# Kernel tuning notes

Measured on AMD Instinct MI355X. Metric: run time of the kernel, lower is better.

The kernel has to match this reference:

```python
import jax, jax.numpy as jnp
import numpy as np

B, D, H, O, E = 8192, 1024, 4096, 1024, 3

def setup_inputs() -> dict:
    key = jax.random.key(0)
    ks = jax.random.split(key, 8)
    s = lambda fan_in: 1.0 / np.sqrt(fan_in)
    return {
        "x":   jax.random.normal(ks[0], (B, D), jnp.float32),
        "gw1": jax.random.normal(ks[1], (D, 256), jnp.float32) * s(D),
        "gb1": jnp.zeros((256,), jnp.float32),
        "gw2": jax.random.normal(ks[2], (256, 128), jnp.float32) * s(256),
        "gb2": jnp.zeros((128,), jnp.float32),
        "gw3": jax.random.normal(ks[3], (128, E), jnp.float32) * s(128),
        "gb3": jnp.zeros((E,), jnp.float32),
        "ew1": jax.random.normal(ks[4], (E, D, H), jnp.float32) * s(D),
        "eb1": jnp.zeros((E, H), jnp.float32),
        "ew2": jax.random.normal(ks[5], (E, H, O), jnp.float32) * s(H),
        "eb2": jnp.zeros((E, O), jnp.float32),
        "top_k": 2,
    }

def reference(x, gw1, gb1, gw2, gb2, gw3, gb3, ew1, eb1, ew2, eb2, top_k):
    # Gating network (dropout is identity in eval mode)
    g = jax.nn.relu(x @ gw1 + gb1)
    g = jax.nn.relu(g @ gw2 + gb2)
    gates = jax.nn.softmax(g @ gw3 + gb3, axis=-1)          # [B, E]

    # top-k routing with renormalized weights
    topk_scores, topk_idx = jax.lax.top_k(gates, top_k)     # [B, k]
    topk_scores = topk_scores / jnp.sum(topk_scores, axis=-1, keepdims=True)

    # scatter normalized scores into dense [B, E] combine weights
    b_ix = jnp.arange(x.shape[0])[:, None]
    combine = jnp.zeros_like(gates).at[b_ix, topk_idx].add(topk_scores)  # [B, E]

    # run all experts densely (small E=3), combine with routing weights
    eh = jax.nn.relu(jnp.einsum('bd,edh->beh', x, ew1) + eb1[None])      # [B, E, H]
    eo = jnp.einsum('beh,eho->beo', eh, ew2) + eb2[None]                 # [B, E, O]
    out = jnp.einsum('be,beo->bo', combine, eo)                          # [B, O]
    return out, gates
```

## Files before the change

### kernel.cpp

```cpp
#include <hip/hip_runtime.h>
#include <cstdint>
#include <cstddef>

#define B_ROWS 8192
#define D_DIM  1024
#define H_DIM  4096
#define O_DIM  1024
#define E_NUM  3
#define K2     (2 * H_DIM)
#define MT256  34
#define SLOT_MAX (MT256 * 256)

typedef __attribute__((ext_vector_type(4))) float f4;
typedef __attribute__((ext_vector_type(8))) _Float16 half8;

__device__ __forceinline__ unsigned short f2h_bits(float f) {
  _Float16 h = (_Float16)f;
  return __builtin_bit_cast(unsigned short, h);
}

__device__ __forceinline__ void async16(const void* g, void* l) {
  __builtin_amdgcn_global_load_lds(
      (const __attribute__((address_space(1))) unsigned int*)g,
      (__attribute__((address_space(3))) unsigned int*)l, 16, 0, 0);
}

__global__ __launch_bounds__(256) void k_cast_x(const float* __restrict__ in,
                                                unsigned short* __restrict__ out) {
  size_t i = (size_t)blockIdx.x * 256 + threadIdx.x;
  const f4* p = (const f4*)in;
  f4 a = p[2 * i], b = p[2 * i + 1];
  half8 h;
#pragma unroll
  for (int j = 0; j < 4; ++j) { h[j] = (_Float16)a[j]; h[4 + j] = (_Float16)b[j]; }
  *(half8*)(out + 8 * i) = h;
}

__global__ __launch_bounds__(256) void k_transpose_cast(const float* __restrict__ in,
                                                        unsigned short* __restrict__ out,
                                                        int R, int C) {
  __shared__ float tile[32][33];
  const size_t eoff = (size_t)blockIdx.z * R * C;
  const float* I = in + eoff;
  unsigned short* O = out + eoff;
  int c0 = blockIdx.x * 32, r0 = blockIdx.y * 32;
  int tx = threadIdx.x & 31, ty = threadIdx.x >> 5;
#pragma unroll
  for (int i = 0; i < 4; ++i)
    tile[ty + 8 * i][tx] = I[(size_t)(r0 + ty + 8 * i) * C + c0 + tx];
  __syncthreads();
#pragma unroll
  for (int i = 0; i < 4; ++i)
    O[(size_t)(c0 + ty + 8 * i) * R + r0 + tx] = f2h_bits(tile[tx][ty + 8 * i]);
}

__global__ __launch_bounds__(256) void k_gemm_f32(const float* __restrict__ A,
                                                  const float* __restrict__ Bm,
                                                  const float* __restrict__ bias,
                                                  float* __restrict__ C,
                                                  int N, int K) {
  __shared__ float sAT[16][68];
  __shared__ float sB[16][68];
  const int t = threadIdx.x;
  const int tx = t & 15, ty = t >> 4;
  const int m0 = blockIdx.y * 64, n0 = blockIdx.x * 64;
  float acc[4][4] = {};
  for (int k0 = 0; k0 < K; k0 += 16) {
    __syncthreads();
#pragma unroll
    for (int i = 0; i < 4; ++i) {
      int idx = t + i * 256;
      int r = idx >> 4, c = idx & 15;
      sAT[c][r] = A[(size_t)(m0 + r) * K + (k0 + c)];
      int rb = idx >> 6, cb = idx & 63;
      sB[rb][cb] = Bm[(size_t)(k0 + rb) * N + (n0 + cb)];
    }
    __syncthreads();
#pragma unroll
    for (int kk = 0; kk < 16; ++kk) {
      f4 av = *(const f4*)&sAT[kk][ty * 4];
      f4 bv = *(const f4*)&sB[kk][tx * 4];
#pragma unroll
      for (int i = 0; i < 4; ++i)
#pragma unroll
        for (int j = 0; j < 4; ++j)
          acc[i][j] = fmaf(av[i], bv[j], acc[i][j]);
    }
  }
#pragma unroll
  for (int i = 0; i < 4; ++i) {
    int row = m0 + ty * 4 + i;
    f4 v;
#pragma unroll
    for (int j = 0; j < 4; ++j)
      v[j] = fmaxf(acc[i][j] + bias[n0 + tx * 4 + j], 0.f);
    *(f4*)&C[(size_t)row * N + n0 + tx * 4] = v;
  }
}

__global__ __launch_bounds__(256) void k_gate_topk(const float* __restrict__ h2,
                                                   const float* __restrict__ gw3,
                                                   const float* __restrict__ gb3,
                                                   float* __restrict__ gates,
                                                   float* __restrict__ combine,
                                                   int* __restrict__ bucket) {
  const int lane = threadIdx.x & 63;
  const int row = blockIdx.x * 4 + (threadIdx.x >> 6);
  const float* h = h2 + (size_t)row * 128;
  float h0 = h[lane], h1 = h[lane + 64];
  float l0 = h0 * gw3[lane * 3 + 0] + h1 * gw3[(lane + 64) * 3 + 0];
  float l1 = h0 * gw3[lane * 3 + 1] + h1 * gw3[(lane + 64) * 3 + 1];
  float l2 = h0 * gw3[lane * 3 + 2] + h1 * gw3[(lane + 64) * 3 + 2];
#pragma unroll
  for (int off = 32; off > 0; off >>= 1) {
    l0 += __shfl_down(l0, off);
    l1 += __shfl_down(l1, off);
    l2 += __shfl_down(l2, off);
  }
  if (lane == 0) {
    float g0 = l0 + gb3[0], g1v = l1 + gb3[1], g2v = l2 + gb3[2];
    float mx = fmaxf(g0, fmaxf(g1v, g2v));
    float e0 = expf(g0 - mx), e1 = expf(g1v - mx), e2 = expf(g2v - mx);
    float inv = 1.f / (e0 + e1 + e2);
    float p0 = e0 * inv, p1 = e1 * inv, p2 = e2 * inv;
    gates[row * 3 + 0] = p0; gates[row * 3 + 1] = p1; gates[row * 3 + 2] = p2;
    int amin = 0; float pm = p0;
    if (p1 <= pm) { pm = p1; amin = 1; }
    if (p2 <= pm) { pm = p2; amin = 2; }
    float denom = (p0 + p1 + p2) - pm;
    combine[row * 3 + 0] = (amin == 0) ? 0.f : p0 / denom;
    combine[row * 3 + 1] = (amin == 1) ? 0.f : p1 / denom;
    combine[row * 3 + 2] = (amin == 2) ? 0.f : p2 / denom;
    bucket[row] = amin;
  }
}

__global__ __launch_bounds__(256) void k_count(const int* __restrict__ bucket,
                                               int* __restrict__ cnt) {
  int row = blockIdx.x * 256 + threadIdx.x;
  int b = bucket[row];
  int lane = threadIdx.x & 63;
#pragma unroll
  for (int bid = 0; bid < 3; ++bid) {
    unsigned long long m = __ballot(b == bid);
    if (m && b == bid) {
      int prefix = __popcll(m & ((1ull << lane) - 1));
      if (prefix == 0) atomicAdd(&cnt[bid], __popcll(m));
    }
  }
}

__global__ void k_meta(const int* __restrict__ cnt, int* __restrict__ meta,
                       int* __restrict__ cnt2) {
  int t0 = (cnt[0] + 255) >> 8;
  int t1 = (cnt[1] + 255) >> 8;
  int t2 = (cnt[2] + 255) >> 8;
  meta[0] = 0; meta[1] = t0; meta[2] = t0 + t1; meta[3] = t0 + t1 + t2;
  cnt2[0] = 0; cnt2[1] = 0; cnt2[2] = 0;
}

__global__ __launch_bounds__(256) void k_scatter(const int* __restrict__ bucket,
                                                 const int* __restrict__ meta,
                                                 int* __restrict__ cnt2,
                                                 int* __restrict__ sorted) {
  int row = blockIdx.x * 256 + threadIdx.x;
  int b = bucket[row];
  int lane = threadIdx.x & 63;
#pragma unroll
  for (int bid = 0; bid < 3; ++bid) {
    unsigned long long m = __ballot(b == bid);
    if (m) {
      int cntm = __popcll(m);
      int leader = __ffsll((unsigned long long)m) - 1;
      int base = 0;
      if (lane == leader) base = atomicAdd(&cnt2[bid], cntm);
      base = __shfl(base, leader);
      if (b == bid) {
        int prefix = __popcll(m & ((1ull << lane) - 1));
        sorted[meta[bid] * 256 + base + prefix] = row;
      }
    }
  }
}

__device__ __forceinline__ void bucket_experts(int b, int& ea, int& eb) {
  ea = (b == 0) ? 1 : 0;
  eb = (b == 2) ? 1 : 2;
}


#define BAR8()  do { __builtin_amdgcn_s_barrier(); __builtin_amdgcn_sched_barrier(0); } while (0)
#define LGKM0() do { asm volatile("s_waitcnt lgkmcnt(0)" ::: "memory"); __builtin_amdgcn_sched_barrier(0); } while (0)
#define VMW(n)  do { asm volatile("s_waitcnt vmcnt(" #n ")" ::: "memory"); __builtin_amdgcn_sched_barrier(0); } while (0)

#define STG_A(buf, h, kt) do { \
    async16(aptr[(h) * 2 + 0] + (size_t)(kt) * 64, smem + (buf) * 32768 + (h) * 16384 + t * 16); \
    async16(aptr[(h) * 2 + 1] + (size_t)(kt) * 64, smem + (buf) * 32768 + (h) * 16384 + 8192 + t * 16); \
  } while (0)
#define STG_B(buf, h, kt) do { \
    async16(bptr[(h) * 2 + 0] + (size_t)(kt) * 64, smem + 65536 + (buf) * 32768 + (h) * 16384 + t * 16); \
    async16(bptr[(h) * 2 + 1] + (size_t)(kt) * 64, smem + 65536 + (buf) * 32768 + (h) * 16384 + 8192 + t * 16); \
  } while (0)
#define LDA8(buf, mh) do { \
    _Pragma("unroll") \
    for (int mf = 0; mf < 4; ++mf) { \
      fa[mf][0] = *(const half8*)(smem + (buf) * 32768 + baseA + (mh) * 8192 + mf * 2048 + ck0); \
      fa[mf][1] = *(const half8*)(smem + (buf) * 32768 + baseA + (mh) * 8192 + mf * 2048 + ck1); \
    } } while (0)
#define LDB8(buf, nh) do { \
    _Pragma("unroll") \
    for (int nf2 = 0; nf2 < 2; ++nf2) { \
      fb[(nh) * 2 + nf2][0] = *(const half8*)(smem + (buf) * 32768 + baseB + ((nh) * 2 + nf2) * 2048 + ck0); \
      fb[(nh) * 2 + nf2][1] = *(const half8*)(smem + (buf) * 32768 + baseB + ((nh) * 2 + nf2) * 2048 + ck1); \
    } } while (0)
#define MM8(mh, nh) do { \
    _Pragma("unroll") \
    for (int mf = 0; mf < 4; ++mf) { \
      _Pragma("unroll") \
      for (int nf2 = 0; nf2 < 2; ++nf2) { \
        acc[(mh) * 4 + mf][(nh) * 2 + nf2] = __builtin_amdgcn_mfma_f32_16x16x32_f16( \
            fa[mf][0], fb[(nh) * 2 + nf2][0], acc[(mh) * 4 + mf][(nh) * 2 + nf2], 0, 0, 0); \
        acc[(mh) * 4 + mf][(nh) * 2 + nf2] = __builtin_amdgcn_mfma_f32_16x16x32_f16( \
            fa[mf][1], fb[(nh) * 2 + nf2][1], acc[(mh) * 4 + mf][(nh) * 2 + nf2], 0, 0, 0); \
      } } } while (0)

#define KLOOP8(NITER, LASTKT) \
  _Pragma("unroll 1") \
  for (int it = 0; it < (NITER) - 1; ++it) { \
    const int kt = 2 * it; \
    LDA8(0, 0); LDB8(0, 0); STG_A(1, 0, kt + 1); \
    BAR8(); LGKM0(); \
    __builtin_amdgcn_s_setprio(1); MM8(0, 0); __builtin_amdgcn_s_setprio(0); \
    BAR8(); \
    LDB8(0, 1); STG_A(1, 1, kt + 1); \
    BAR8(); LGKM0(); \
    __builtin_amdgcn_s_setprio(1); MM8(0, 1); __builtin_amdgcn_s_setprio(0); \
    BAR8(); \
    LDA8(0, 1); STG_B(0, 0, kt + 2); \
    BAR8(); LGKM0(); \
    __builtin_amdgcn_s_setprio(1); MM8(1, 0); __builtin_amdgcn_s_setprio(0); \
    BAR8(); \
    STG_A(0, 0, kt + 2); \
    BAR8(); LGKM0(); \
    __builtin_amdgcn_s_setprio(1); MM8(1, 1); __builtin_amdgcn_s_setprio(0); \
    VMW(4); BAR8(); \
    LDA8(1, 0); LDB8(1, 0); STG_A(0, 1, kt + 2); \
    BAR8(); LGKM0(); \
    __builtin_amdgcn_s_setprio(1); MM8(0, 0); __builtin_amdgcn_s_setprio(0); \
    BAR8(); \
    LDB8(1, 1); STG_B(0, 1, kt + 2); \
    BAR8(); LGKM0(); \
    __builtin_amdgcn_s_setprio(1); MM8(0, 1); __builtin_amdgcn_s_setprio(0); \
    BAR8(); \
    LDA8(1, 1); STG_B(1, 0, kt + 3); \
    BAR8(); LGKM0(); \
    __builtin_amdgcn_s_setprio(1); MM8(1, 0); __builtin_amdgcn_s_setprio(0); \
    BAR8(); \
    STG_B(1, 1, kt + 3); \
    BAR8(); LGKM0(); \
    __builtin_amdgcn_s_setprio(1); MM8(1, 1); __builtin_amdgcn_s_setprio(0); \
    VMW(4); BAR8(); \
  } \
  {  \
    LDA8(0, 0); LDB8(0, 0); STG_A(1, 0, LASTKT); \
    BAR8(); LGKM0(); \
    __builtin_amdgcn_s_setprio(1); MM8(0, 0); __builtin_amdgcn_s_setprio(0); \
    BAR8(); \
    LDB8(0, 1); STG_A(1, 1, LASTKT); \
    BAR8(); LGKM0(); \
    __builtin_amdgcn_s_setprio(1); MM8(0, 1); __builtin_amdgcn_s_setprio(0); \
    BAR8(); \
    LDA8(0, 1); \
    BAR8(); LGKM0(); \
    __builtin_amdgcn_s_setprio(1); MM8(1, 0); __builtin_amdgcn_s_setprio(0); \
    BAR8(); \
    BAR8(); LGKM0(); \
    __builtin_amdgcn_s_setprio(1); MM8(1, 1); __builtin_amdgcn_s_setprio(0); \
    VMW(0); BAR8(); \
    LDA8(1, 0); LDB8(1, 0); MM8(0, 0); \
    LDB8(1, 1); MM8(0, 1); \
    LDA8(1, 1); MM8(1, 0); \
    MM8(1, 1); \
  }

__global__ __launch_bounds__(512, 2) void k_expert_h8(const unsigned short* __restrict__ Xh,
                                                      const unsigned short* __restrict__ W1T,
                                                      const float* __restrict__ combine,
                                                      const float* __restrict__ eb1,
                                                      const int* __restrict__ sorted,
                                                      const int* __restrict__ meta,
                                                      unsigned short* __restrict__ EHS) {
  constexpr int K = D_DIM;
  const int mt = blockIdx.x;
  const int tb1 = meta[1], tb2 = meta[2], tb3 = meta[3];
  if (mt >= tb3) return;
  const int b = (mt >= tb2) ? 2 : (mt >= tb1) ? 1 : 0;
  int ea, ebx; bucket_experts(b, ea, ebx);
  const int z = blockIdx.z;
  const int e = z ? ebx : ea;
  const int slot0 = mt * 256;
  const int n0 = blockIdx.y * 256;

  __shared__ __align__(16) char smem[131072];
  __shared__ float sC[256];
  const int t = threadIdx.x;
  if (t < 256) {
    int r = sorted[slot0 + t];
    sC[t] = (r < 0) ? 0.f : combine[(size_t)r * 3 + e];
  }

  const int jrow = t >> 3;
  const int j = (t & 7) ^ (jrow & 7);
  const unsigned short* aptr[4];
  const unsigned short* bptr[4];
#pragma unroll
  for (int i = 0; i < 4; ++i) {
    int R = jrow + i * 64;
    int r = sorted[slot0 + R];
    int rr = (r < 0) ? 0 : r;
    aptr[i] = Xh + (size_t)rr * K + j * 8;
    bptr[i] = W1T + (size_t)e * H_DIM * K + (size_t)(n0 + R) * K + j * 8;
  }
  const int lane = t & 63;
  const int wid = t >> 6;
  const int wm = wid >> 2, wn = wid & 3;
  const int quad = lane >> 4, l16 = lane & 15;
  const int ck0 = ((quad) ^ (l16 & 7)) * 16;
  const int ck1 = ((4 + quad) ^ (l16 & 7)) * 16;
  const int baseA = (wm * 128 + l16) * 128;
  const int baseB = 65536 + (wn * 64 + l16) * 128;

  f4 acc[8][4] = {};
  half8 fa[4][2], fb[4][2];

  STG_A(0, 0, 0); STG_A(0, 1, 0); STG_B(0, 0, 0); STG_B(0, 1, 0);
  STG_B(1, 0, 1); STG_B(1, 1, 1);
  VMW(4); BAR8();

  KLOOP8(8, 15)

  const float* bias = eb1 + (size_t)e * H_DIM;
#pragma unroll
  for (int nf = 0; nf < 4; ++nf) {
    int col = n0 + wn * 64 + nf * 16 + l16;
    float bb = bias[col];
#pragma unroll
    for (int mf = 0; mf < 8; ++mf) {
#pragma unroll
      for (int r = 0; r < 4; ++r) {
        int rloc = wm * 128 + mf * 16 + quad * 4 + r;
        float v = fmaxf(acc[mf][nf][r] + bb, 0.f) * sC[rloc];
        EHS[(size_t)(slot0 + rloc) * K2 + (size_t)z * H_DIM + col] = f2h_bits(v);
      }
    }
  }
}

__global__ __launch_bounds__(512, 2) void k_expert_o8(const unsigned short* __restrict__ EHS,
                                                      const unsigned short* __restrict__ W2T,
                                                      const float* __restrict__ combine,
                                                      const float* __restrict__ eb2,
                                                      const int* __restrict__ sorted,
                                                      const int* __restrict__ meta,
                                                      float* __restrict__ OUT) {
  const int mt = blockIdx.x;
  const int tb1 = meta[1], tb2 = meta[2], tb3 = meta[3];
  if (mt >= tb3) return;
  const int b = (mt >= tb2) ? 2 : (mt >= tb1) ? 1 : 0;
  int ea, ebx; bucket_experts(b, ea, ebx);
  const int hz = blockIdx.z;
  const int e = hz ? ebx : ea;
  const int slot0 = mt * 256;
  const int n0 = blockIdx.y * 256;

  __shared__ __align__(16) char smem[131072];
  __shared__ int sRow[256];
  __shared__ float sCa[256], sCb[256];
  const int t = threadIdx.x;
  if (t < 256) {
    int r = sorted[slot0 + t];
    sRow[t] = r;
    int rr = (r < 0) ? 0 : r;
    sCa[t] = combine[(size_t)rr * 3 + ea];
    sCb[t] = combine[(size_t)rr * 3 + ebx];
  }

  const int jrow = t >> 3;
  const int j = (t & 7) ^ (jrow & 7);
  const unsigned short* aptr[4];
  const unsigned short* bptr[4];
#pragma unroll
  for (int i = 0; i < 4; ++i) {
    int R = jrow + i * 64;
    int r = sorted[slot0 + R];
    int rr = (r < 0) ? 0 : r;
    aptr[i] = EHS + (size_t)(slot0 + R) * K2 + (size_t)hz * H_DIM + j * 8;
    (void)rr;
    bptr[i] = W2T + (size_t)e * O_DIM * H_DIM + (size_t)(n0 + R) * H_DIM + j * 8;
  }
  const int lane = t & 63;
  const int wid = t >> 6;
  const int wm = wid >> 2, wn = wid & 3;
  const int quad = lane >> 4, l16 = lane & 15;
  const int ck0 = ((quad) ^ (l16 & 7)) * 16;
  const int ck1 = ((4 + quad) ^ (l16 & 7)) * 16;
  const int baseA = (wm * 128 + l16) * 128;
  const int baseB = 65536 + (wn * 64 + l16) * 128;

  f4 acc[8][4] = {};
  half8 fa[4][2], fb[4][2];

  STG_A(0, 0, 0); STG_A(0, 1, 0); STG_B(0, 0, 0); STG_B(0, 1, 0);
  STG_B(1, 0, 1); STG_B(1, 1, 1);
  VMW(4); BAR8();

  KLOOP8(32, 63)

#pragma unroll
  for (int nf = 0; nf < 4; ++nf) {
    int col = n0 + wn * 64 + nf * 16 + l16;
    float ba = eb2[(size_t)ea * O_DIM + col];
    float bb = eb2[(size_t)ebx * O_DIM + col];
#pragma unroll
    for (int mf = 0; mf < 8; ++mf) {
#pragma unroll
      for (int r = 0; r < 4; ++r) {
        int rloc = wm * 128 + mf * 16 + quad * 4 + r;
        int rowg = sRow[rloc];
        if (rowg >= 0) {
          float v = acc[mf][nf][r];
          if (hz == 0) v += sCa[rloc] * ba + sCb[rloc] * bb;
          atomicAdd(&OUT[(size_t)rowg * O_DIM + col], v);
        }
      }
    }
  }
}

extern "C" void kernel_launch(void* const* d_in, const int* in_sizes, int n_in,
                              void* d_out, int out_size, void* d_ws, size_t ws_size,
                              hipStream_t stream) {
  const float* x   = (const float*)d_in[0];
  const float* gw1 = (const float*)d_in[1];
  const float* gb1 = (const float*)d_in[2];
  const float* gw2 = (const float*)d_in[3];
  const float* gb2 = (const float*)d_in[4];
  const float* gw3 = (const float*)d_in[5];
  const float* gb3 = (const float*)d_in[6];
  const float* ew1 = (const float*)d_in[7];
  const float* eb1 = (const float*)d_in[8];
  const float* ew2 = (const float*)d_in[9];
  const float* eb2 = (const float*)d_in[10];
  float* out = (float*)d_out;
  float* gates = out + (size_t)B_ROWS * O_DIM;

  char* ws = (char*)d_ws;
  size_t off = 0;
  auto take = [&](size_t bytes) -> char* {
    char* p = ws + off;
    off += (bytes + 255) & ~(size_t)255;
    return p;
  };
  unsigned short* xh  = (unsigned short*)take((size_t)B_ROWS * D_DIM * 2);
  unsigned short* w1t = (unsigned short*)take((size_t)E_NUM * H_DIM * D_DIM * 2);
  unsigned short* w2t = (unsigned short*)take((size_t)E_NUM * O_DIM * H_DIM * 2);
  float* comb   = (float*)take((size_t)B_ROWS * 3 * 4);
  float* g1     = (float*)take((size_t)B_ROWS * 256 * 4);
  float* h2     = (float*)take((size_t)B_ROWS * 128 * 4);
  int* bucket   = (int*)take((size_t)B_ROWS * 4);
  int* sorted   = (int*)take((size_t)SLOT_MAX * 4);
  int* cnt      = (int*)take(3 * 4);
  int* cnt2     = (int*)take(3 * 4);
  int* meta     = (int*)take(4 * 4);
  unsigned short* ehs = (unsigned short*)take((size_t)SLOT_MAX * K2 * 2);

  hipMemsetAsync(cnt, 0, 3 * 4, stream);
  hipMemsetAsync(sorted, 0xFF, (size_t)SLOT_MAX * 4, stream);
  hipMemsetAsync(out, 0, (size_t)B_ROWS * O_DIM * 4, stream);

  k_cast_x<<<dim3(B_ROWS * D_DIM / (256 * 8)), 256, 0, stream>>>(x, xh);
  k_transpose_cast<<<dim3(H_DIM / 32, D_DIM / 32, E_NUM), 256, 0, stream>>>(ew1, w1t, D_DIM, H_DIM);
  k_transpose_cast<<<dim3(O_DIM / 32, H_DIM / 32, E_NUM), 256, 0, stream>>>(ew2, w2t, H_DIM, O_DIM);

  k_gemm_f32<<<dim3(256 / 64, B_ROWS / 64), 256, 0, stream>>>(x, gw1, gb1, g1, 256, D_DIM);
  k_gemm_f32<<<dim3(128 / 64, B_ROWS / 64), 256, 0, stream>>>(g1, gw2, gb2, h2, 128, 256);
  k_gate_topk<<<dim3(B_ROWS / 4), 256, 0, stream>>>(h2, gw3, gb3, gates, comb, bucket);

  k_count<<<dim3(B_ROWS / 256), 256, 0, stream>>>(bucket, cnt);
  k_meta<<<1, 1, 0, stream>>>(cnt, meta, cnt2);
  k_scatter<<<dim3(B_ROWS / 256), 256, 0, stream>>>(bucket, meta, cnt2, sorted);

  k_expert_h8<<<dim3(MT256, H_DIM / 256, 2), 512, 0, stream>>>(
      xh, w1t, comb, eb1, sorted, meta, ehs);
  k_expert_o8<<<dim3(MT256, O_DIM / 256, 2), 512, 0, stream>>>(
      ehs, w2t, comb, eb2, sorted, meta, out);
}
```

Measured before the change: 743.1 us.

## Fuse the two gating-MLP layers into one kernel, keeping hidden activations in LDS

Replaces the two separate fp32 GEMM launches for the gating network with a single kernel. Each 512-thread block computes a 32-row tile of relu(x@gw1+b1), keeps the 256-wide hidden result in shared memory, and immediately computes the second layer. This removes the g1 round-trip through global memory and one launch. The cost is that gw1 is now re-read per 32-row tile instead of per 64x64 tile, and there are fewer, larger blocks (256 blocks). A dead load in the expert output kernel is also removed.

```diff
diff --git a/kernel.cpp b/kernel.cpp
--- a/kernel.cpp
+++ b/kernel.cpp
@@ -54,26 +54,31 @@
     O[(size_t)(c0 + ty + 8 * i) * R + r0 + tx] = f2h_bits(tile[tx][ty + 8 * i]);
 }
 
-__global__ __launch_bounds__(256) void k_gemm_f32(const float* __restrict__ A,
-                                                  const float* __restrict__ Bm,
-                                                  const float* __restrict__ bias,
-                                                  float* __restrict__ C,
-                                                  int N, int K) {
-  __shared__ float sAT[16][68];
-  __shared__ float sB[16][68];
+__global__ __launch_bounds__(512) void k_gate12(const float* __restrict__ x,
+                                                const float* __restrict__ gw1,
+                                                const float* __restrict__ gb1,
+                                                const float* __restrict__ gw2,
+                                                const float* __restrict__ gb2,
+                                                float* __restrict__ h2out) {
+  __shared__ float g1t[32][264];
+  __shared__ float sB[16][260];
+  __shared__ float sAT[16][36];
   const int t = threadIdx.x;
-  const int tx = t & 15, ty = t >> 4;
-  const int m0 = blockIdx.y * 64, n0 = blockIdx.x * 64;
+  const int m0 = blockIdx.x * 32;
+
+  const int ty = t >> 6, tx = t & 63;
   float acc[4][4] = {};
-  for (int k0 = 0; k0 < K; k0 += 16) {
+  for (int k0 = 0; k0 < D_DIM; k0 += 16) {
     __syncthreads();
-#pragma unroll
-    for (int i = 0; i < 4; ++i) {
-      int idx = t + i * 256;
-      int r = idx >> 4, c = idx & 15;
-      sAT[c][r] = A[(size_t)(m0 + r) * K + (k0 + c)];
-      int rb = idx >> 6, cb = idx & 63;
-      sB[rb][cb] = Bm[(size_t)(k0 + rb) * N + (n0 + cb)];
+    {
+      int r = t >> 4, c = t & 15;
+      sAT[c][r] = x[(size_t)(m0 + r) * D_DIM + k0 + c];
+    }
+#pragma unroll
+    for (int i = 0; i < 8; ++i) {
+      int idx = t + i * 512;
+      int rb = idx >> 8, cb = idx & 255;
+      sB[rb][cb] = gw1[(size_t)(k0 + rb) * 256 + cb];
     }
     __syncthreads();
 #pragma unroll
@@ -87,14 +92,47 @@
           acc[i][j] = fmaf(av[i], bv[j], acc[i][j]);
     }
   }
+  __syncthreads();
 #pragma unroll
   for (int i = 0; i < 4; ++i) {
-    int row = m0 + ty * 4 + i;
     f4 v;
 #pragma unroll
     for (int j = 0; j < 4; ++j)
-      v[j] = fmaxf(acc[i][j] + bias[n0 + tx * 4 + j], 0.f);
-    *(f4*)&C[(size_t)row * N + n0 + tx * 4] = v;
+      v[j] = fmaxf(acc[i][j] + gb1[tx * 4 + j], 0.f);
+    *(f4*)&g1t[ty * 4 + i][tx * 4] = v;
+  }
+
+  const int ty2 = t >> 5, tx2 = t & 31;
+  float acc2[2][4] = {};
+  for (int k0 = 0; k0 < 256; k0 += 16) {
+    __syncthreads();
+#pragma unroll
+    for (int i = 0; i < 4; ++i) {
+      int idx = t + i * 512;
+      int rb = idx >> 7, cb = idx & 127;
+      sB[rb][cb] = gw2[(size_t)(k0 + rb) * 128 + cb];
+    }
+    __syncthreads();
+#pragma unroll
+    for (int kk = 0; kk < 16; ++kk) {
+      float a0 = g1t[ty2 * 2 + 0][k0 + kk];
+      float a1 = g1t[ty2 * 2 + 1][k0 + kk];
+      f4 bv = *(const f4*)&sB[kk][tx2 * 4];
+#pragma unroll
+      for (int j = 0; j < 4; ++j) {
+        acc2[0][j] = fmaf(a0, bv[j], acc2[0][j]);
+        acc2[1][j] = fmaf(a1, bv[j], acc2[1][j]);
+      }
+    }
+  }
+#pragma unroll
+  for (int i = 0; i < 2; ++i) {
+    int row = m0 + ty2 * 2 + i;
+    f4 v;
+#pragma unroll
+    for (int j = 0; j < 4; ++j)
+      v[j] = fmaxf(acc2[i][j] + gb2[tx2 * 4 + j], 0.f);
+    *(f4*)&h2out[(size_t)row * 128 + tx2 * 4] = v;
   }
 }
 
@@ -392,10 +430,7 @@
 #pragma unroll
   for (int i = 0; i < 4; ++i) {
     int R = jrow + i * 64;
-    int r = sorted[slot0 + R];
-    int rr = (r < 0) ? 0 : r;
     aptr[i] = EHS + (size_t)(slot0 + R) * K2 + (size_t)hz * H_DIM + j * 8;
-    (void)rr;
     bptr[i] = W2T + (size_t)e * O_DIM * H_DIM + (size_t)(n0 + R) * H_DIM + j * 8;
   }
   const int lane = t & 63;
@@ -465,7 +500,6 @@
   unsigned short* w1t = (unsigned short*)take((size_t)E_NUM * H_DIM * D_DIM * 2);
   unsigned short* w2t = (unsigned short*)take((size_t)E_NUM * O_DIM * H_DIM * 2);
   float* comb   = (float*)take((size_t)B_ROWS * 3 * 4);
-  float* g1     = (float*)take((size_t)B_ROWS * 256 * 4);
   float* h2     = (float*)take((size_t)B_ROWS * 128 * 4);
   int* bucket   = (int*)take((size_t)B_ROWS * 4);
   int* sorted   = (int*)take((size_t)SLOT_MAX * 4);
@@ -482,8 +516,7 @@
   k_transpose_cast<<<dim3(H_DIM / 32, D_DIM / 32, E_NUM), 256, 0, stream>>>(ew1, w1t, D_DIM, H_DIM);
   k_transpose_cast<<<dim3(O_DIM / 32, H_DIM / 32, E_NUM), 256, 0, stream>>>(ew2, w2t, H_DIM, O_DIM);
 
-  k_gemm_f32<<<dim3(256 / 64, B_ROWS / 64), 256, 0, stream>>>(x, gw1, gb1, g1, 256, D_DIM);
-  k_gemm_f32<<<dim3(128 / 64, B_ROWS / 64), 256, 0, stream>>>(g1, gw2, gb2, h2, 128, 256);
+  k_gate12<<<dim3(B_ROWS / 32), 512, 0, stream>>>(x, gw1, gb1, gw2, gb2, h2);
   k_gate_topk<<<dim3(B_ROWS / 4), 256, 0, stream>>>(h2, gw3, gb3, gates, comb, bucket);
 
   k_count<<<dim3(B_ROWS / 256), 256, 0, stream>>>(bucket, cnt);
```

Result: slower. 773.3 us (+4.1%).
